# Optimization experiments

Measured on AMD Instinct MI355X. Metric: run time of the kernel, lower is better.

Reference implementation:

```python
import jax, jax.numpy as jnp
import numpy as np

B, N, D, H = 8, 1025, 768, 12
PRE = 1            # prefix (CLS) tokens
P = N - PRE        # patch tokens
HD = D // H
EPS = 1e-6


def setup_inputs() -> dict:
    key = jax.random.key(0)
    ks = jax.random.split(key, 8)
    x = jax.random.normal(ks[0], (B, N, D), dtype=jnp.float32)
    graph = jax.random.uniform(ks[1], (B, P, P), dtype=jnp.float32)
    transferability = jax.random.uniform(ks[2], (B, P), dtype=jnp.float32)
    Wqkv = jax.random.normal(ks[3], (3 * D, D), dtype=jnp.float32) * 0.02
    bqkv = jnp.zeros((3 * D,), dtype=jnp.float32)
    Wproj = jax.random.normal(ks[4], (D, D), dtype=jnp.float32) * 0.02
    bproj = jnp.zeros((D,), dtype=jnp.float32)
    return {"x": x, "graph": graph, "transferability": transferability,
            "Wqkv": Wqkv, "bqkv": bqkv, "Wproj": Wproj, "bproj": bproj,
            "prefix_tokens": PRE}


def _build_mask(graph, transferability, prefix_tokens, n_tokens):
    # patch_weights: [B, P]
    pw = transferability / (jnp.sum(transferability, axis=1, keepdims=True) + EPS)
    b, p = pw.shape
    pre = prefix_tokens
    # Block layout: [[1s (pre,pre), pw broadcast (pre,P)], [pw[:,None] (P,pre), graph]]
    top_left = jnp.ones((b, pre, pre), dtype=graph.dtype)
    top_right = jnp.broadcast_to(pw[:, None, :], (b, pre, p))
    bot_left = jnp.broadcast_to(pw[:, :, None], (b, p, pre))
    top = jnp.concatenate([top_left, top_right], axis=2)
    bot = jnp.concatenate([bot_left, graph], axis=2)
    return jnp.concatenate([top, bot], axis=1)  # [B, N, N]


def reference(x, graph, transferability, Wqkv, bqkv, Wproj, bproj, prefix_tokens):
    bsz, n, d = x.shape
    scale = HD ** -0.5
    qkv = x @ Wqkv.T + bqkv                          # [B, N, 3D]
    qkv = qkv.reshape(bsz, n, 3, H, HD).transpose(2, 0, 3, 1, 4)  # [3, B, H, N, hd]
    q, k, v = qkv[0], qkv[1], qkv[2]
    attn = jax.nn.softmax(jnp.einsum('bhid,bhjd->bhij', q, k) * scale, axis=-1)
    mask = _build_mask(graph, transferability, prefix_tokens, n)  # [B, N, N]
    attn = attn * mask[:, None, :, :]
    attn = attn / (jnp.sum(attn, axis=-1, keepdims=True) + EPS)
    out = jnp.einsum('bhij,bhjd->bhid', attn, v)     # [B, H, N, hd]
    out = out.transpose(0, 2, 1, 3).reshape(bsz, n, d)
    return out @ Wproj.T + bproj
```

## Files before the change

### kernel.cpp

```cpp
#include <hip/hip_runtime.h>
#include <stdint.h>

constexpr int Bq = 8, Nn = 1025, Dd = 768, Hh = 12, HDd = 64, Pp = 1024;
constexpr int NP = 1088;
constexpr int MROWS = Bq * Nn;
constexpr float EPSI = 1e-6f;

typedef __attribute__((ext_vector_type(8))) short bfrag;
typedef __attribute__((ext_vector_type(4))) float ffrag;
typedef __attribute__((ext_vector_type(4))) float f4;
typedef __attribute__((ext_vector_type(4))) unsigned short us4;

#define MFMA16(a, b, c) __builtin_amdgcn_mfma_f32_16x16x32_bf16((a), (b), (c), 0, 0, 0)

#if __has_builtin(__builtin_amdgcn_exp2f)
#define EXP2(x) __builtin_amdgcn_exp2f(x)
#else
#define EXP2(x) exp2f(x)
#endif

__device__ __forceinline__ unsigned short f2bf(float f) {
  union { float f; uint32_t u; } v{f};
  uint32_t u = v.u;
  return (unsigned short)((u + 0x7fffu + ((u >> 16) & 1u)) >> 16);
}
__device__ __forceinline__ float bf2f(unsigned short s) {
  union { uint32_t u; float f; } v; v.u = ((uint32_t)s) << 16; return v.f;
}
__device__ __forceinline__ uint32_t pkbf(float a, float b) {
  uint32_t r;
  asm("v_cvt_pk_bf16_f32 %0, %1, %2" : "=v"(r) : "v"(a), "v"(b));
  return r;
}

__device__ __forceinline__ void gload16(const void* g, void* l) {
  __builtin_amdgcn_global_load_lds((const __attribute__((address_space(1))) unsigned int*)g,
                                   (__attribute__((address_space(3))) unsigned int*)l, 16, 0, 0);
}

__global__ __launch_bounds__(256) void conv_kernel(const float* __restrict__ src,
                                                   unsigned short* __restrict__ dst, int n4) {
  int idx = blockIdx.x * blockDim.x + threadIdx.x;
  int stride = gridDim.x * blockDim.x;
  for (int i = idx; i < n4; i += stride) {
    f4 v = ((const f4*)src)[i];
    us4 o; o[0] = f2bf(v[0]); o[1] = f2bf(v[1]); o[2] = f2bf(v[2]); o[3] = f2bf(v[3]);
    ((us4*)dst)[i] = o;
  }
}

__global__ __launch_bounds__(256) void pw_kernel(const float* __restrict__ tr, float* __restrict__ pw) {
  int b = blockIdx.x;
  __shared__ float red[256];
  float s = 0.f;
  for (int j = threadIdx.x; j < Pp; j += 256) s += tr[b * Pp + j];
  red[threadIdx.x] = s; __syncthreads();
  for (int o = 128; o > 0; o >>= 1) { if (threadIdx.x < o) red[threadIdx.x] += red[threadIdx.x + o]; __syncthreads(); }
  float inv = 1.f / (red[0] + EPSI);
  for (int j = threadIdx.x; j < Pp; j += 256) pw[b * Pp + j] = tr[b * Pp + j] * inv;
}

__global__ __launch_bounds__(256) void mask_kernel(const float* __restrict__ graph,
                                                   const float* __restrict__ pw,
                                                   unsigned short* __restrict__ mask) {
  int i = blockIdx.x, b = blockIdx.y;
  unsigned short* mrow = mask + ((size_t)b * NP + i) * NP;
  if (i >= Nn) { for (int j = threadIdx.x; j < NP; j += 256) mrow[j] = 0; return; }
  if (i == 0) {
    for (int j = threadIdx.x; j < NP; j += 256) {
      float v = (j == 0) ? 1.f : (j <= Pp ? pw[b * Pp + j - 1] : 0.f);
      mrow[j] = f2bf(v);
    }
  } else {
    const float* grow = graph + ((size_t)b * Pp + (i - 1)) * Pp;
    for (int j = threadIdx.x; j < NP; j += 256) {
      float v = (j == 0) ? pw[b * Pp + i - 1] : (j <= Pp ? grow[j - 1] : 0.f);
      mrow[j] = f2bf(v);
    }
  }
}

__global__ __launch_bounds__(256) void padzero_kernel(unsigned short* __restrict__ Qo,
                                                      unsigned short* __restrict__ Ko,
                                                      unsigned short* __restrict__ Vo) {
  int bh = blockIdx.x;
  unsigned short* qp = Qo + ((size_t)bh * NP + Nn) * 64;
  unsigned short* kp = Ko + ((size_t)bh * NP + Nn) * 64;
  for (int idx = threadIdx.x; idx < (NP - Nn) * 64; idx += 256) { qp[idx] = 0; kp[idx] = 0; }
  unsigned short* vp = Vo + (size_t)bh * 64 * NP;
  for (int idx = threadIdx.x; idx < 64 * (NP - Nn); idx += 256) {
    int d = idx / (NP - Nn), j = Nn + (idx - d * (NP - Nn));
    vp[(size_t)d * NP + j] = 0;
  }
}

__device__ __forceinline__ void gemm_main(const unsigned short* __restrict__ A, int rowA0, int rowAmax,
                                          const unsigned short* __restrict__ Bw, int rowB0,
                                          uint4* lds, ffrag acc[4][4], int tid) {
  const int l = tid & 63, lm = l & 15, lg = l >> 4, w = tid >> 6, wr = w >> 1, wc = w & 1;
  const unsigned short* aS[4]; const unsigned short* bS[4];
#pragma unroll
  for (int q = 0; q < 4; q++) {
    int c = tid + 256 * q, r = c >> 3, p = c & 7, g = p ^ (r & 7);
    int ra = rowA0 + r; if (ra > rowAmax) ra = rowAmax;
    aS[q] = A + (size_t)ra * 768 + 8 * g;
    bS[q] = Bw + (size_t)(rowB0 + r) * 768 + 8 * g;
  }
  uint4* buf0 = lds;
  uint4* buf1 = lds + 2048;
#pragma unroll
  for (int q = 0; q < 4; q++) {
    gload16(aS[q], buf0 + tid + 256 * q);
    gload16(bS[q], buf0 + 1024 + tid + 256 * q);
    aS[q] += 64; bS[q] += 64;
  }
  asm volatile("s_waitcnt vmcnt(0)" ::: "memory");
  __builtin_amdgcn_sched_barrier(0);
  __builtin_amdgcn_s_barrier();
#pragma unroll 1
  for (int kt = 0; kt < 12; kt++) {
    uint4* cur = (kt & 1) ? buf1 : buf0;
    uint4* nxt = (kt & 1) ? buf0 : buf1;
    if (kt < 11) {
#pragma unroll
      for (int q = 0; q < 4; q++) {
        gload16(aS[q], nxt + tid + 256 * q);
        gload16(bS[q], nxt + 1024 + tid + 256 * q);
        aS[q] += 64; bS[q] += 64;
      }
    }
    const bfrag* LA = (const bfrag*)cur;
    const bfrag* LB = (const bfrag*)(cur + 1024);
    bfrag af[4][2], bf_[4][2];
#pragma unroll
    for (int am = 0; am < 4; am++) {
      int row = wr * 64 + am * 16 + lm;
      af[am][0] = LA[row * 8 + ((0 + lg) ^ (row & 7))];
      af[am][1] = LA[row * 8 + ((4 + lg) ^ (row & 7))];
    }
#pragma unroll
    for (int an = 0; an < 4; an++) {
      int row = wc * 64 + an * 16 + lm;
      bf_[an][0] = LB[row * 8 + ((0 + lg) ^ (row & 7))];
      bf_[an][1] = LB[row * 8 + ((4 + lg) ^ (row & 7))];
    }
#pragma unroll
    for (int am = 0; am < 4; am++)
#pragma unroll
      for (int an = 0; an < 4; an++) {
        acc[am][an] = MFMA16(af[am][0], bf_[an][0], acc[am][an]);
        acc[am][an] = MFMA16(af[am][1], bf_[an][1], acc[am][an]);
      }
    asm volatile("s_waitcnt vmcnt(0)" ::: "memory");
    __builtin_amdgcn_sched_barrier(0);
    __builtin_amdgcn_s_barrier();
  }
}

__device__ __forceinline__ int xcd_chunk_map(int orig, int nwg) {
  int qq = nwg >> 3, rr = nwg & 7;
  int xcd = orig & 7, idx = orig >> 3;
  int base = (xcd < rr) ? xcd * (qq + 1) : rr * (qq + 1) + (xcd - rr) * qq;
  return base + idx;
}

__global__ __launch_bounds__(256) void qkv_gemm_kernel(const unsigned short* __restrict__ X,
                                                       const unsigned short* __restrict__ W,
                                                       const float* __restrict__ bias,
                                                       unsigned short* __restrict__ Qo,
                                                       unsigned short* __restrict__ Ko,
                                                       unsigned short* __restrict__ Vo) {
  __shared__ uint4 lds[4096];
  int tid = threadIdx.x;
  int wg = xcd_chunk_map(blockIdx.x, 65 * 18);
  int xt = wg / 18, yt = wg - 18 * xt;
  ffrag zero4 = {0.f, 0.f, 0.f, 0.f};
  ffrag acc[4][4];
#pragma unroll
  for (int i = 0; i < 4; i++)
#pragma unroll
    for (int j = 0; j < 4; j++) acc[i][j] = zero4;
  gemm_main(X, xt * 128, MROWS - 1, W, yt * 128, lds, acc, tid);
  const int l = tid & 63, lm = l & 15, lg = l >> 4, w = tid >> 6, wr = w >> 1, wc = w & 1;
#pragma unroll
  for (int an = 0; an < 4; an++) {
    int gc = yt * 128 + wc * 64 + an * 16 + lm;
    int which = gc / 768, rr = gc - which * 768, h = rr >> 6, hd = rr & 63;
    float bv = bias[gc];
#pragma unroll
    for (int am = 0; am < 4; am++) {
      int grb = xt * 128 + wr * 64 + am * 16 + 4 * lg;
#pragma unroll
      for (int r = 0; r < 4; r++) {
        int gr = grb + r;
        if (gr >= MROWS) continue;
        int b = gr / Nn, i = gr - b * Nn;
        size_t bh = (size_t)(b * Hh + h);
        float v = acc[am][an][r] + bv;
        if (which == 0)      Qo[(bh * NP + i) * 64 + hd] = f2bf(v * 0.18033688f);
        else if (which == 1) Ko[(bh * NP + i) * 64 + hd] = f2bf(v);
        else                 Vo[(bh * 64 + hd) * NP + i] = f2bf(v);
      }
    }
  }
}

__global__ __launch_bounds__(256) void proj_gemm_kernel(const unsigned short* __restrict__ A,
                                                        const unsigned short* __restrict__ W,
                                                        const float* __restrict__ bias,
                                                        float* __restrict__ out) {
  __shared__ uint4 lds[4096];
  int tid = threadIdx.x;
  int wg = xcd_chunk_map(blockIdx.x, 65 * 6);
  int xt = wg / 6, yt = wg - 6 * xt;
  ffrag zero4 = {0.f, 0.f, 0.f, 0.f};
  ffrag acc[4][4];
#pragma unroll
  for (int i = 0; i < 4; i++)
#pragma unroll
    for (int j = 0; j < 4; j++) acc[i][j] = zero4;
  gemm_main(A, xt * 128, MROWS - 1, W, yt * 128, lds, acc, tid);
  const int l = tid & 63, lm = l & 15, lg = l >> 4, w = tid >> 6, wr = w >> 1, wc = w & 1;
#pragma unroll
  for (int an = 0; an < 4; an++) {
    int gc = yt * 128 + wc * 64 + an * 16 + lm;
    float bv = bias[gc];
#pragma unroll
    for (int am = 0; am < 4; am++) {
      int grb = xt * 128 + wr * 64 + am * 16 + 4 * lg;
#pragma unroll
      for (int r = 0; r < 4; r++) {
        int gr = grb + r;
        if (gr >= MROWS) continue;
        out[(size_t)gr * 768 + gc] = acc[am][an][r] + bv;
      }
    }
  }
}

__global__ __launch_bounds__(256) void attn_kernel(const unsigned short* __restrict__ Qg,
                                                   const unsigned short* __restrict__ Kg,
                                                   const unsigned short* __restrict__ Vg,
                                                   const unsigned short* __restrict__ Mg,
                                                   unsigned short* __restrict__ Og) {
  __shared__ uint4 smem[1536];
  int tid = threadIdx.x, w = tid >> 6, l = tid & 63, lm = l & 15, lg = l >> 4;
  int bx = blockIdx.x;
  int b = bx & 7, t5 = bx >> 3;
  int h = t5 % 12, ib = t5 / 12;
  size_t bh = (size_t)(b * Hh + h);
  const unsigned short* Qb = Qg + bh * NP * 64;
  const unsigned short* Kb = Kg + bh * NP * 64;
  const unsigned short* Vb = Vg + bh * 64 * NP;
  int i0 = ib * 64 + w * 16;
  int irow = i0 + lm;
  const unsigned short* Mrow = Mg + (size_t)b * NP * NP + (size_t)irow * NP;

  bfrag qf0 = *(const bfrag*)(Qb + (size_t)irow * 64 + 8 * lg);
  bfrag qf1 = *(const bfrag*)(Qb + (size_t)irow * 64 + 32 + 8 * lg);

  ffrag zero4 = {0.f, 0.f, 0.f, 0.f};
  ffrag oacc[4] = {zero4, zero4, zero4, zero4};
  float Zp = 0.f, Tp = 0.f;

  int rS = tid >> 3, pS = tid & 7, gS = pS ^ (rS & 7);
  const unsigned short* kS = Kb + rS * 64 + 8 * gS;
  const unsigned short* vS = Vb + (size_t)rS * NP + 8 * gS;
  uint4* ldsK4 = smem; uint4* ldsV4 = smem + 512;
  char* Pbase = (char*)(smem + 1024) + w * 2048;
  const bfrag* LK = (const bfrag*)ldsK4;
  const bfrag* LV = (const bfrag*)ldsV4;

#pragma unroll 1
  for (int t = 0; t < 17; t++) {
    uint4 k0 = *(const uint4*)kS, k1 = *(const uint4*)(kS + 2048);
    uint4 v0 = *(const uint4*)vS, v1 = *(const uint4*)(vS + 32 * NP);
    int j0 = t * 64;
    us4 mv[4];
#pragma unroll
    for (int jm = 0; jm < 4; jm++) mv[jm] = *(const us4*)(Mrow + j0 + 16 * jm + 4 * lg);
    __syncthreads();
    ldsK4[tid] = k0; ldsK4[tid + 256] = k1; ldsV4[tid] = v0; ldsV4[tid + 256] = v1;
    __syncthreads();
    kS += 64 * 64; vS += 64;

    ffrag s[4];
#pragma unroll
    for (int jm = 0; jm < 4; jm++) {
      int row = jm * 16 + lm;
      bfrag a0 = LK[row * 8 + ((0 + lg) ^ (row & 7))];
      bfrag a1 = LK[row * 8 + ((4 + lg) ^ (row & 7))];
      ffrag a = zero4;
      a = MFMA16(a0, qf0, a);
      a = MFMA16(a1, qf1, a);
      s[jm] = a;
    }
#pragma unroll
    for (int jm = 0; jm < 4; jm++) {
      float p0 = EXP2(s[jm][0]), p1 = EXP2(s[jm][1]), p2 = EXP2(s[jm][2]), p3 = EXP2(s[jm][3]);
      Zp += (p0 + p1) + (p2 + p3);
      float q0 = p0 * bf2f(mv[jm][0]), q1 = p1 * bf2f(mv[jm][1]);
      float q2 = p2 * bf2f(mv[jm][2]), q3 = p3 * bf2f(mv[jm][3]);
      Tp += (q0 + q1) + (q2 + q3);
      uint2 pk; pk.x = pkbf(q0, q1); pk.y = pkbf(q2, q3);
      int cpos = (((jm << 1) | (lg >> 1)) ^ (lm & 7));
      *(uint2*)(Pbase + lm * 128 + cpos * 16 + 8 * (lg & 1)) = pk;
    }
#pragma unroll
    for (int ks = 0; ks < 2; ks++) {
      bfrag pa = *(const bfrag*)(Pbase + lm * 128 + ((((ks << 2) | lg)) ^ (lm & 7)) * 16);
#pragma unroll
      for (int dm = 0; dm < 4; dm++) {
        int vrow = dm * 16 + lm;
        bfrag vb = LV[vrow * 8 + ((ks * 4 + lg) ^ (vrow & 7))];
        oacc[dm] = MFMA16(pa, vb, oacc[dm]);
      }
    }
  }
  Zp += __shfl_xor(Zp, 16); Zp += __shfl_xor(Zp, 32);
  Tp += __shfl_xor(Tp, 16); Tp += __shfl_xor(Tp, 32);
  float dn_row = 1.f / (Tp + EPSI * Zp);
  float dn[4];
#pragma unroll
  for (int r = 0; r < 4; r++) dn[r] = __shfl(dn_row, 4 * lg + r);
#pragma unroll
  for (int dm = 0; dm < 4; dm++)
#pragma unroll
    for (int r = 0; r < 4; r++) {
      int i = i0 + 4 * lg + r;
      if (i < Nn) Og[((size_t)(b * Nn + i)) * Dd + h * 64 + dm * 16 + lm] = f2bf(oacc[dm][r] * dn[r]);
    }
}

extern "C" void kernel_launch(void* const* d_in, const int* in_sizes, int n_in,
                              void* d_out, int out_size, void* d_ws, size_t ws_size,
                              hipStream_t stream) {
  const float* x      = (const float*)d_in[0];
  const float* graph  = (const float*)d_in[1];
  const float* transf = (const float*)d_in[2];
  const float* Wqkv   = (const float*)d_in[3];
  const float* bqkv   = (const float*)d_in[4];
  const float* Wproj  = (const float*)d_in[5];
  const float* bproj  = (const float*)d_in[6];
  float* out = (float*)d_out;
  char* ws = (char*)d_ws;

  unsigned short* xbf  = (unsigned short*)(ws + 0);
  unsigned short* wqb  = (unsigned short*)(ws + 12595200);
  unsigned short* wpb  = (unsigned short*)(ws + 16134144);
  unsigned short* Qb   = (unsigned short*)(ws + 17313792);
  unsigned short* Kb   = (unsigned short*)(ws + 30683136);
  unsigned short* Vb   = (unsigned short*)(ws + 44052480);
  float*          pw   = (float*)(ws + 57421824);
  unsigned short* mask = (unsigned short*)(ws + 57454592);
  unsigned short* aob  = xbf;

  conv_kernel<<<2048, 256, 0, stream>>>(x, xbf, (MROWS * Dd) / 4);
  conv_kernel<<<1728, 256, 0, stream>>>(Wqkv, wqb, (3 * Dd * Dd) / 4);
  conv_kernel<<<576, 256, 0, stream>>>(Wproj, wpb, (Dd * Dd) / 4);
  pw_kernel<<<Bq, 256, 0, stream>>>(transf, pw);
  mask_kernel<<<dim3(NP, Bq), 256, 0, stream>>>(graph, pw, mask);
  padzero_kernel<<<96, 256, 0, stream>>>(Qb, Kb, Vb);
  qkv_gemm_kernel<<<65 * 18, 256, 0, stream>>>(xbf, wqb, bqkv, Qb, Kb, Vb);
  attn_kernel<<<1632, 256, 0, stream>>>(Qb, Kb, Vb, mask, aob);
  proj_gemm_kernel<<<65 * 6, 256, 0, stream>>>(aob, wpb, bproj, out);
}
```

Before: 206.1 us.

## Double-buffer K/V tiles via direct global-to-LDS loads and prefetch mask

The attention kernel now double-buffers its K/V tiles in shared memory, using direct global-to-LDS loads (gload16). The loads and the mask reads for the next tile are issued before computing on the current one, so each iteration needs one barrier instead of two register-staged syncs. It also raises wave priority around the MFMA sections and drops the Z accumulator, so the eps term in the denominator is no longer computed. LDS use grows to 40KB per block, which may lower occupancy, and removing eps*Z slightly changes numerics.

Result: no change. 205.3 us (-0.3%).

```diff
diff --git a/kernel.cpp b/kernel.cpp
--- a/kernel.cpp
+++ b/kernel.cpp
@@ -243,7 +243,7 @@
                                                    const unsigned short* __restrict__ Vg,
                                                    const unsigned short* __restrict__ Mg,
                                                    unsigned short* __restrict__ Og) {
-  __shared__ uint4 smem[1536];
+  __shared__ uint4 smem[2560];
   int tid = threadIdx.x, w = tid >> 6, l = tid & 63, lm = l & 15, lg = l >> 4;
   int bx = blockIdx.x;
   int b = bx & 7, t5 = bx >> 3;
@@ -261,30 +261,47 @@
 
   ffrag zero4 = {0.f, 0.f, 0.f, 0.f};
   ffrag oacc[4] = {zero4, zero4, zero4, zero4};
-  float Zp = 0.f, Tp = 0.f;
-
-  int rS = tid >> 3, pS = tid & 7, gS = pS ^ (rS & 7);
-  const unsigned short* kS = Kb + rS * 64 + 8 * gS;
-  const unsigned short* vS = Vb + (size_t)rS * NP + 8 * gS;
-  uint4* ldsK4 = smem; uint4* ldsV4 = smem + 512;
-  char* Pbase = (char*)(smem + 1024) + w * 2048;
-  const bfrag* LK = (const bfrag*)ldsK4;
-  const bfrag* LV = (const bfrag*)ldsV4;
+  float Tp = 0.f;
+
+  int rS = tid >> 3, pS = tid & 7;
+  int rS2 = rS + 32;
+  const unsigned short* kS0 = Kb + (size_t)rS * 64 + 8 * (pS ^ (rS & 7));
+  const unsigned short* kS1 = Kb + (size_t)rS2 * 64 + 8 * (pS ^ (rS2 & 7));
+  const unsigned short* vS0 = Vb + (size_t)rS * NP + 8 * (pS ^ (rS & 7));
+  const unsigned short* vS1 = Vb + (size_t)rS2 * NP + 8 * (pS ^ (rS2 & 7));
+
+  char* Pbase = (char*)(smem + 2048) + w * 2048;
+
+  gload16(kS0, smem + tid);
+  gload16(kS1, smem + tid + 256);
+  gload16(vS0, smem + 1024 + tid);
+  gload16(vS1, smem + 1024 + tid + 256);
+  us4 mva[4], mvb[4];
+#pragma unroll
+  for (int jm = 0; jm < 4; jm++) mva[jm] = *(const us4*)(Mrow + 16 * jm + 4 * lg);
+  asm volatile("s_waitcnt vmcnt(0)" ::: "memory");
+  __builtin_amdgcn_sched_barrier(0);
+  __builtin_amdgcn_s_barrier();
 
 #pragma unroll 1
   for (int t = 0; t < 17; t++) {
-    uint4 k0 = *(const uint4*)kS, k1 = *(const uint4*)(kS + 2048);
-    uint4 v0 = *(const uint4*)vS, v1 = *(const uint4*)(vS + 32 * NP);
-    int j0 = t * 64;
-    us4 mv[4];
-#pragma unroll
-    for (int jm = 0; jm < 4; jm++) mv[jm] = *(const us4*)(Mrow + j0 + 16 * jm + 4 * lg);
-    __syncthreads();
-    ldsK4[tid] = k0; ldsK4[tid + 256] = k1; ldsV4[tid] = v0; ldsV4[tid + 256] = v1;
-    __syncthreads();
-    kS += 64 * 64; vS += 64;
+    int cb = (t & 1) << 9;
+    if (t < 16) {
+      int nb = ((t + 1) & 1) << 9;
+      size_t ko = (size_t)(t + 1) * 4096;
+      int vo = (t + 1) * 64;
+      gload16(kS0 + ko, smem + nb + tid);
+      gload16(kS1 + ko, smem + nb + tid + 256);
+      gload16(vS0 + vo, smem + 1024 + nb + tid);
+      gload16(vS1 + vo, smem + 1024 + nb + tid + 256);
+#pragma unroll
+      for (int jm = 0; jm < 4; jm++) mvb[jm] = *(const us4*)(Mrow + (t + 1) * 64 + 16 * jm + 4 * lg);
+    }
+    const bfrag* LK = (const bfrag*)(smem + cb);
+    const bfrag* LV = (const bfrag*)(smem + 1024 + cb);
 
     ffrag s[4];
+    __builtin_amdgcn_s_setprio(1);
 #pragma unroll
     for (int jm = 0; jm < 4; jm++) {
       int row = jm * 16 + lm;
@@ -295,17 +312,18 @@
       a = MFMA16(a1, qf1, a);
       s[jm] = a;
     }
+    __builtin_amdgcn_s_setprio(0);
 #pragma unroll
     for (int jm = 0; jm < 4; jm++) {
       float p0 = EXP2(s[jm][0]), p1 = EXP2(s[jm][1]), p2 = EXP2(s[jm][2]), p3 = EXP2(s[jm][3]);
-      Zp += (p0 + p1) + (p2 + p3);
-      float q0 = p0 * bf2f(mv[jm][0]), q1 = p1 * bf2f(mv[jm][1]);
-      float q2 = p2 * bf2f(mv[jm][2]), q3 = p3 * bf2f(mv[jm][3]);
+      float q0 = p0 * bf2f(mva[jm][0]), q1 = p1 * bf2f(mva[jm][1]);
+      float q2 = p2 * bf2f(mva[jm][2]), q3 = p3 * bf2f(mva[jm][3]);
       Tp += (q0 + q1) + (q2 + q3);
       uint2 pk; pk.x = pkbf(q0, q1); pk.y = pkbf(q2, q3);
       int cpos = (((jm << 1) | (lg >> 1)) ^ (lm & 7));
       *(uint2*)(Pbase + lm * 128 + cpos * 16 + 8 * (lg & 1)) = pk;
     }
+    __builtin_amdgcn_s_setprio(1);
 #pragma unroll
     for (int ks = 0; ks < 2; ks++) {
       bfrag pa = *(const bfrag*)(Pbase + lm * 128 + ((((ks << 2) | lg)) ^ (lm & 7)) * 16);
@@ -316,10 +334,15 @@
         oacc[dm] = MFMA16(pa, vb, oacc[dm]);
       }
     }
-  }
-  Zp += __shfl_xor(Zp, 16); Zp += __shfl_xor(Zp, 32);
+    __builtin_amdgcn_s_setprio(0);
+#pragma unroll
+    for (int jm = 0; jm < 4; jm++) mva[jm] = mvb[jm];
+    asm volatile("s_waitcnt vmcnt(0)" ::: "memory");
+    __builtin_amdgcn_sched_barrier(0);
+    __builtin_amdgcn_s_barrier();
+  }
   Tp += __shfl_xor(Tp, 16); Tp += __shfl_xor(Tp, 32);
-  float dn_row = 1.f / (Tp + EPSI * Zp);
+  float dn_row = 1.f / Tp;
   float dn[4];
 #pragma unroll
   for (int r = 0; r < 4; r++) dn[r] = __shfl(dn_row, 4 * lg + r);
```

## Load K/V fragments directly from global memory, drop LDS staging and Z sum

Applied to the files above, without the earlier changes.

Removes the shared-memory staging of K and V tiles and the two block-wide barriers per iteration; each wave now reads its MFMA operand fragments directly from global/L2. It also drops the softmax denominator Z accumulation, approximating the final normalization as 1/T and ignoring the eps*Z term. It adds s_setprio around the MFMA sections. The cost is redundant global loads across the four waves, which share K/V but no longer share them through LDS, and a small numerical deviation from the eps term.

Result: slower. 388.5 us (+88.5%).

```diff
diff --git a/kernel.cpp b/kernel.cpp
--- a/kernel.cpp
+++ b/kernel.cpp
@@ -243,7 +243,7 @@
                                                    const unsigned short* __restrict__ Vg,
                                                    const unsigned short* __restrict__ Mg,
                                                    unsigned short* __restrict__ Og) {
-  __shared__ uint4 smem[1536];
+  __shared__ uint4 smem[512];
   int tid = threadIdx.x, w = tid >> 6, l = tid & 63, lm = l & 15, lg = l >> 4;
   int bx = blockIdx.x;
   int b = bx & 7, t5 = bx >> 3;
@@ -261,65 +261,57 @@
 
   ffrag zero4 = {0.f, 0.f, 0.f, 0.f};
   ffrag oacc[4] = {zero4, zero4, zero4, zero4};
-  float Zp = 0.f, Tp = 0.f;
-
-  int rS = tid >> 3, pS = tid & 7, gS = pS ^ (rS & 7);
-  const unsigned short* kS = Kb + rS * 64 + 8 * gS;
-  const unsigned short* vS = Vb + (size_t)rS * NP + 8 * gS;
-  uint4* ldsK4 = smem; uint4* ldsV4 = smem + 512;
-  char* Pbase = (char*)(smem + 1024) + w * 2048;
-  const bfrag* LK = (const bfrag*)ldsK4;
-  const bfrag* LV = (const bfrag*)ldsV4;
+  float Tp = 0.f;
+
+  char* Pbase = (char*)smem + w * 2048;
+
+  const unsigned short* Krow = Kb + (size_t)lm * 64 + 8 * lg;
+  const unsigned short* Vrow = Vb + (size_t)lm * NP;
 
 #pragma unroll 1
   for (int t = 0; t < 17; t++) {
-    uint4 k0 = *(const uint4*)kS, k1 = *(const uint4*)(kS + 2048);
-    uint4 v0 = *(const uint4*)vS, v1 = *(const uint4*)(vS + 32 * NP);
     int j0 = t * 64;
-    us4 mv[4];
-#pragma unroll
-    for (int jm = 0; jm < 4; jm++) mv[jm] = *(const us4*)(Mrow + j0 + 16 * jm + 4 * lg);
-    __syncthreads();
-    ldsK4[tid] = k0; ldsK4[tid + 256] = k1; ldsV4[tid] = v0; ldsV4[tid + 256] = v1;
-    __syncthreads();
-    kS += 64 * 64; vS += 64;
+    us4 mva[4];
+#pragma unroll
+    for (int jm = 0; jm < 4; jm++) mva[jm] = *(const us4*)(Mrow + j0 + 16 * jm + 4 * lg);
 
     ffrag s[4];
+    __builtin_amdgcn_s_setprio(1);
 #pragma unroll
     for (int jm = 0; jm < 4; jm++) {
-      int row = jm * 16 + lm;
-      bfrag a0 = LK[row * 8 + ((0 + lg) ^ (row & 7))];
-      bfrag a1 = LK[row * 8 + ((4 + lg) ^ (row & 7))];
+      const unsigned short* kp = Krow + (size_t)(j0 + jm * 16) * 64;
+      bfrag a0 = *(const bfrag*)(kp);
+      bfrag a1 = *(const bfrag*)(kp + 32);
       ffrag a = zero4;
       a = MFMA16(a0, qf0, a);
       a = MFMA16(a1, qf1, a);
       s[jm] = a;
     }
+    __builtin_amdgcn_s_setprio(0);
 #pragma unroll
     for (int jm = 0; jm < 4; jm++) {
       float p0 = EXP2(s[jm][0]), p1 = EXP2(s[jm][1]), p2 = EXP2(s[jm][2]), p3 = EXP2(s[jm][3]);
-      Zp += (p0 + p1) + (p2 + p3);
-      float q0 = p0 * bf2f(mv[jm][0]), q1 = p1 * bf2f(mv[jm][1]);
-      float q2 = p2 * bf2f(mv[jm][2]), q3 = p3 * bf2f(mv[jm][3]);
+      float q0 = p0 * bf2f(mva[jm][0]), q1 = p1 * bf2f(mva[jm][1]);
+      float q2 = p2 * bf2f(mva[jm][2]), q3 = p3 * bf2f(mva[jm][3]);
       Tp += (q0 + q1) + (q2 + q3);
       uint2 pk; pk.x = pkbf(q0, q1); pk.y = pkbf(q2, q3);
       int cpos = (((jm << 1) | (lg >> 1)) ^ (lm & 7));
       *(uint2*)(Pbase + lm * 128 + cpos * 16 + 8 * (lg & 1)) = pk;
     }
+    __builtin_amdgcn_s_setprio(1);
 #pragma unroll
     for (int ks = 0; ks < 2; ks++) {
       bfrag pa = *(const bfrag*)(Pbase + lm * 128 + ((((ks << 2) | lg)) ^ (lm & 7)) * 16);
 #pragma unroll
       for (int dm = 0; dm < 4; dm++) {
-        int vrow = dm * 16 + lm;
-        bfrag vb = LV[vrow * 8 + ((ks * 4 + lg) ^ (vrow & 7))];
+        bfrag vb = *(const bfrag*)(Vrow + (size_t)dm * 16 * NP + j0 + 8 * (ks * 4 + lg));
         oacc[dm] = MFMA16(pa, vb, oacc[dm]);
       }
     }
-  }
-  Zp += __shfl_xor(Zp, 16); Zp += __shfl_xor(Zp, 32);
+    __builtin_amdgcn_s_setprio(0);
+  }
   Tp += __shfl_xor(Tp, 16); Tp += __shfl_xor(Tp, 32);
-  float dn_row = 1.f / (Tp + EPSI * Zp);
+  float dn_row = 1.f / Tp;
   float dn[4];
 #pragma unroll
   for (int r = 0; r < 4; r++) dn[r] = __shfl(dn_row, 4 * lg + r);
```
